# Optimization experiments

Hardware: AMD Instinct MI355X
Metric: run time of the kernel (lower is better)

## Reference

```python
import jax, jax.numpy as jnp
import numpy as np

B_J0 = 0.01
BETA = 1.8   # isAdapt=1
LENS = 0.5
DT = 1.0
IN_SIZE = 1
STRIDE = IN_SIZE
T = 784 // STRIDE
HID = (512, 512, 512)
OUT = 10
N = 256


def _create_general_mask(dim, c_min, c_max, min_dc, max_dc, phase_max, T):
    # faithful port of ASRNN_general.create_general_mask (numpy, static)
    dcs = np.linspace(min_dc, max_dc, dim)
    cycles = np.linspace(c_min, c_max, dim)
    shifts = np.linspace(0.0, float(int(phase_max * c_max)), dim)
    rows = []
    for cyc, dc, ps in zip(cycles, dcs, shifts):
        cyc = int(np.round(cyc))
        on = int(np.round(dc * cyc))
        pat = [1.0] * on + [0.0] * (cyc - on)
        ps = int(np.round(ps))
        if ps > 0:
            pat = pat[-ps:] + pat[:-ps]
        rows.append(pat * (T // cyc) + pat[: T % cyc])
    return np.asarray(rows, dtype=np.float32)  # [dim, T]

MASK1 = jnp.asarray(_create_general_mask(HID[0], 2, 8, 0.2, 0.8, 0.5, T))
MASK2 = jnp.asarray(_create_general_mask(HID[1], 4, 16, 0.2, 0.8, 0.5, T))
MASK3 = jnp.asarray(_create_general_mask(HID[2], 8, 32, 0.2, 0.8, 0.5, T))

# per-step input gather indices (faithful to the start_idx branch in forward)
_starts = np.arange(T) * STRIDE
_IDX = np.where(_starts[:, None] < T - IN_SIZE,
                _starts[:, None] + np.arange(IN_SIZE)[None, :],
                (784 - IN_SIZE) + np.arange(IN_SIZE)[None, :])  # [T, IN]


@jax.custom_vjp
def act_fun(x):
    return (x > 0.0).astype(x.dtype)

def _act_fwd(x):
    return (x > 0.0).astype(x.dtype), x

def _act_bwd(x, g):
    return (g * (jnp.abs(x) < LENS).astype(g.dtype),)

act_fun.defvjp(_act_fwd, _act_bwd)


def _mem_update(inputs, mem, spike, tau_adp, b, tau_m, mask_t):
    alpha = jnp.exp(-DT / tau_m)
    ro = jnp.exp(-DT / tau_adp)
    b_new = ro * b + (1.0 - ro) * spike
    Bth = B_J0 + BETA * b_new
    mem_new = mem * alpha + (1.0 - alpha) * inputs - Bth * spike * DT
    mem_new = jnp.where(mask_t == 0.0, mem, mem_new)
    spike_new = act_fun(mem_new - Bth) * mask_t
    return mem_new, spike_new, b_new


def _forward(x, wi1, bi1, wh1, bh1, wi2, bi2, wh2, bh2, wi3, bi3, wo, bo,
             tau_adp1, tau_adp2, tau_adp3, tau_m1, tau_m2, tau_m3):
    n = x.shape[0]
    x_seq = jnp.transpose(x[:, _IDX], (1, 0, 2))            # [T, N, IN]
    pre1 = jnp.einsum('tni,hi->tnh', x_seq, wi1) + bi1       # [T, N, H1]

    def step_fn(carry, xs):
        mem1, spk1, b1, mem2, spk2, b2, mem3, spk3, b3, out_sum, s1, s2, s3 = carry
        p1, m1, m2, m3 = xs
        h1_in = p1 + spk1 @ wh1.T + bh1
        mem1, spk1, b1 = _mem_update(h1_in, mem1, spk1, tau_adp1, b1, tau_m1, m1)
        h2_in = spk1 @ wi2.T + bi2 + spk2 @ wh2.T + bh2
        mem2, spk2, b2 = _mem_update(h2_in, mem2, spk2, tau_adp2, b2, tau_m2, m2)
        h3_in = spk2 @ wi3.T + bi3
        mem3, spk3, b3 = _mem_update(h3_in, mem3, spk3, tau_adp3, b3, tau_m3, m3)
        out_sum = out_sum + spk3 @ wo.T + bo
        return (mem1, spk1, b1, mem2, spk2, b2, mem3, spk3, b3,
                out_sum, s1 + spk1, s2 + spk2, s3 + spk3), None

    z = lambda h: jnp.zeros((n, h), x.dtype)
    f = lambda h: jnp.full((n, h), B_J0, x.dtype)
    carry0 = (z(HID[0]), z(HID[0]), f(HID[0]),
              z(HID[1]), z(HID[1]), f(HID[1]),
              z(HID[2]), z(HID[2]), f(HID[2]),
              jnp.zeros((n, OUT), x.dtype), z(HID[0]), z(HID[1]), z(HID[2]))
    xs = (pre1, MASK1.T, MASK2.T, MASK3.T)
    carry, _ = jax.lax.scan(step_fn, carry0, xs)
    out_sum, s1, s2, s3 = carry[9], carry[10], carry[11], carry[12]
    outputs = out_sum / T
    layer_fr = jnp.stack([s1.sum() / (n * HID[0] * T),
                          s2.sum() / (n * HID[1] * T),
                          s3.sum() / (n * HID[2] * T)])
    return outputs, s1 / T, s2 / T, s3 / T, layer_fr


def setup_inputs() -> dict:
    key = jax.random.key(0)
    ks = jax.random.split(key, 20)
    def xav(k, shp):
        fan_in, fan_out = shp[1], shp[0]
        s = np.sqrt(2.0 / (fan_in + fan_out))
        return jax.random.normal(k, shp, jnp.float32) * s
    return {
        'x': jax.random.uniform(ks[0], (N, 784), jnp.float32),
        'wi1': xav(ks[1], (HID[0], IN_SIZE)), 'bi1': jnp.zeros((HID[0],), jnp.float32),
        'wh1': xav(ks[2], (HID[0], HID[0])), 'bh1': jnp.zeros((HID[0],), jnp.float32),
        'wi2': xav(ks[3], (HID[1], HID[0])), 'bi2': jnp.zeros((HID[1],), jnp.float32),
        'wh2': xav(ks[4], (HID[1], HID[1])), 'bh2': jnp.zeros((HID[1],), jnp.float32),
        'wi3': xav(ks[5], (HID[2], HID[1])), 'bi3': jnp.zeros((HID[2],), jnp.float32),
        'wo': xav(ks[6], (OUT, HID[2])), 'bo': jnp.zeros((OUT,), jnp.float32),
        'tau_adp1': 700.0 + 25.0 * jax.random.normal(ks[7], (HID[0],), jnp.float32),
        'tau_adp2': 700.0 + 25.0 * jax.random.normal(ks[8], (HID[1],), jnp.float32),
        'tau_adp3': 700.0 + 25.0 * jax.random.normal(ks[9], (HID[2],), jnp.float32),
        'tau_m1': 5.0 + jax.random.normal(ks[10], (HID[0],), jnp.float32),
        'tau_m2': 5.0 + jax.random.normal(ks[11], (HID[1],), jnp.float32),
        'tau_m3': 5.0 + jax.random.normal(ks[12], (HID[2],), jnp.float32),
    }


def reference(x, wi1, bi1, wh1, bh1, wi2, bi2, wh2, bh2, wi3, bi3, wo, bo,
              tau_adp1, tau_adp2, tau_adp3, tau_m1, tau_m2, tau_m3):
    return _forward(x, wi1, bi1, wh1, bh1, wi2, bi2, wh2, bh2, wi3, bi3, wo, bo,
                    tau_adp1, tau_adp2, tau_adp3, tau_m1, tau_m2, tau_m3)
```

## Files before the change

kernel.cpp:

```cpp
#include <hip/hip_runtime.h>
#include <stdint.h>

#pragma clang fp contract(off)


static constexpr int    TS      = 784;
static constexpr size_t WS_WT1  = 0;
static constexpr size_t WS_WT2A = 1u << 20;
static constexpr size_t WS_WT2B = 2u << 20;
static constexpr size_t WS_WT3  = 3u << 20;
static constexpr size_t WS_M1   = 4u << 20;
static constexpr size_t WS_M2   = WS_M1 + (size_t)TS * 512;
static constexpr size_t WS_M3   = WS_M2 + (size_t)TS * 512;
static constexpr size_t WS_FRP  = WS_M3 + (size_t)TS * 512;

__device__ __forceinline__ float exp_np(float x) {
  float q = rintf(x * 1.442695040f);
  float r = __fmaf_rn(-q, 0.693359375f, x);
  r = __fmaf_rn(-q, -2.12194440e-4f, r);
  float r2 = r * r;
  float p = 1.9875691500e-4f;
  p = __fmaf_rn(p, r, 1.3981999507e-3f);
  p = __fmaf_rn(p, r, 8.3334519073e-3f);
  p = __fmaf_rn(p, r, 4.1665795894e-2f);
  p = __fmaf_rn(p, r, 1.6666665459e-1f);
  p = __fmaf_rn(p, r, 5.0000001201e-1f);
  p = __fmaf_rn(p, r2, r);
  p = p + 1.0f;
  return ldexpf(p, (int)q);
}

__device__ __forceinline__ int mask_val(int l, int h, int t) {
  const double cmin = (l == 0) ? 2.0 : ((l == 1) ? 4.0 : 8.0);
  const double cmax = (l == 0) ? 8.0 : ((l == 1) ? 16.0 : 32.0);
  const double smax = (l == 0) ? 4.0 : ((l == 1) ? 8.0 : 16.0);
  const double cD = (cmax - cmin) / 511.0;
  const double dD = (0.8 - 0.2) / 511.0;
  const double sD = smax / 511.0;
  const double hd = (double)h;
  double cycd = (h == 511) ? cmax : __dadd_rn(cmin, __dmul_rn(hd, cD));
  double dcd  = (h == 511) ? 0.8  : __dadd_rn(0.2,  __dmul_rn(hd, dD));
  double psd  = (h == 511) ? smax : __dmul_rn(hd, sD);
  int cyc = __double2int_rn(cycd);
  int on  = __double2int_rn(__dmul_rn(dcd, (double)cyc));
  int ps  = __double2int_rn(psd);
  int eff = (ps >= cyc) ? 0 : ps;
  int pos = (t % cyc) - eff;
  if (pos < 0) pos += cyc;
  return (pos < on) ? 1 : 0;
}

__global__ void setup_masks(char* __restrict__ ws) {
  const int t = blockIdx.x, tid = threadIdx.x;
  uint8_t* m1 = (uint8_t*)(ws + WS_M1);
  uint8_t* m2 = (uint8_t*)(ws + WS_M2);
  uint8_t* m3 = (uint8_t*)(ws + WS_M3);
  for (int h = tid; h < 512; h += 256) {
    m1[t * 512 + h] = (uint8_t)mask_val(0, h, t);
    m2[t * 512 + h] = (uint8_t)mask_val(1, h, t);
    m3[t * 512 + h] = (uint8_t)mask_val(2, h, t);
  }
}

__global__ void transpose_kernel(const float* __restrict__ wh1,
                                 const float* __restrict__ wi2,
                                 const float* __restrict__ wh2,
                                 const float* __restrict__ wi3,
                                 char* __restrict__ ws) {
  const int k = blockIdx.x;
  const int m = blockIdx.y;
  const float* W = (m == 0) ? wh1 : (m == 1) ? wi2 : (m == 2) ? wh2 : wi3;
  float* T = (float*)(ws + (size_t)m * (1u << 20));
  for (int j = threadIdx.x; j < 512; j += 256)
    T[(size_t)k * 512 + j] = W[(size_t)j * 512 + k];
}

__device__ __forceinline__ uint32_t upd32(float hin, uint32_t mk, uint32_t osp,
                                          float al, float om, float r, float omr,
                                          float& memv, float& bv) {
  float t1 = r * bv;
  float bn = osp ? (t1 + omr) : t1;
  float bt = 1.8f * bn;
  float Bth = 0.01f + bt;
  float m1 = memv * al;
  float m2 = om * hin;
  float m3 = m1 + m2;
  float mn = osp ? (m3 - Bth) : m3;
  if (!mk) mn = memv;
  uint32_t sn = (mk && (mn - Bth) > 0.0f) ? 1u : 0u;
  memv = mn; bv = bn;
  return sn;
}

__device__ __forceinline__ int expand_list(const uint64_t* __restrict__ bm,
                                           uint32_t mysp, int h,
                                           ushort* __restrict__ kl) {
  const int wh = h >> 6, bpos = h & 63;
  int cnt = 0, rank = 0;
#pragma unroll
  for (int w = 0; w < 8; ++w) {
    uint64_t v = bm[w];
    int pc = __builtin_popcountll(v);
    if (w < wh) rank += pc;
    cnt += pc;
  }
  rank += __builtin_popcountll(bm[wh] & ((1ull << bpos) - 1ull));
  if (mysp) kl[rank] = (ushort)h;
  return cnt;
}

__device__ __forceinline__ float gather_from(const float* __restrict__ base,
                                             const ushort* kl, int from, int cnt,
                                             float s) {
  int i = from;
  for (; i + 16 <= cnt; i += 16) {
    float w0  = base[(size_t)kl[i + 0]  << 9];
    float w1  = base[(size_t)kl[i + 1]  << 9];
    float w2  = base[(size_t)kl[i + 2]  << 9];
    float w3  = base[(size_t)kl[i + 3]  << 9];
    float w4  = base[(size_t)kl[i + 4]  << 9];
    float w5  = base[(size_t)kl[i + 5]  << 9];
    float w6  = base[(size_t)kl[i + 6]  << 9];
    float w7  = base[(size_t)kl[i + 7]  << 9];
    float w8  = base[(size_t)kl[i + 8]  << 9];
    float w9  = base[(size_t)kl[i + 9]  << 9];
    float w10 = base[(size_t)kl[i + 10] << 9];
    float w11 = base[(size_t)kl[i + 11] << 9];
    float w12 = base[(size_t)kl[i + 12] << 9];
    float w13 = base[(size_t)kl[i + 13] << 9];
    float w14 = base[(size_t)kl[i + 14] << 9];
    float w15 = base[(size_t)kl[i + 15] << 9];
    s = s + w0;  s = s + w1;  s = s + w2;  s = s + w3;
    s = s + w4;  s = s + w5;  s = s + w6;  s = s + w7;
    s = s + w8;  s = s + w9;  s = s + w10; s = s + w11;
    s = s + w12; s = s + w13; s = s + w14; s = s + w15;
  }
  for (; i + 4 <= cnt; i += 4) {
    float w0 = base[(size_t)kl[i + 0] << 9];
    float w1 = base[(size_t)kl[i + 1] << 9];
    float w2 = base[(size_t)kl[i + 2] << 9];
    float w3 = base[(size_t)kl[i + 3] << 9];
    s = s + w0; s = s + w1; s = s + w2; s = s + w3;
  }
  for (; i < cnt; ++i) s = s + base[(size_t)kl[i] << 9];
  return s;
}

__global__ __launch_bounds__(512, 1) void rnn_block(
    const float* __restrict__ x,
    const float* __restrict__ wi1, const float* __restrict__ bi1,
    const float* __restrict__ bh1,
    const float* __restrict__ bi2, const float* __restrict__ bh2,
    const float* __restrict__ bi3,
    const float* __restrict__ wo, const float* __restrict__ bo,
    const float* __restrict__ ta1, const float* __restrict__ ta2,
    const float* __restrict__ ta3, const float* __restrict__ tm1,
    const float* __restrict__ tm2, const float* __restrict__ tm3,
    char* __restrict__ ws, float* __restrict__ d_out) {
  const int n = blockIdx.x;
  const int h = threadIdx.x;
  const float* WT1  = (const float*)(ws + WS_WT1);
  const float* WT2A = (const float*)(ws + WS_WT2A);
  const float* WT2B = (const float*)(ws + WS_WT2B);
  const float* WT3  = (const float*)(ws + WS_WT3);
  const uint8_t* M1 = (const uint8_t*)(ws + WS_M1);
  const uint8_t* M2 = (const uint8_t*)(ws + WS_M2);
  const uint8_t* M3 = (const uint8_t*)(ws + WS_M3);

  __shared__ uint64_t bm1s[8], bm2s[8], bm3s[8];
  __shared__ ushort kl1s[512], kl2s[512];
  __shared__ float woS[10 * 513];
  __shared__ double red[512];

  for (int i = h; i < 5120; i += 512) woS[(i / 512) * 513 + (i % 512)] = wo[i];

  float al1 = exp_np(-1.0f / tm1[h]), om1 = 1.0f - al1;
  float ro1 = exp_np(-1.0f / ta1[h]), omr1 = 1.0f - ro1;
  float al2 = exp_np(-1.0f / tm2[h]), om2 = 1.0f - al2;
  float ro2 = exp_np(-1.0f / ta2[h]), omr2 = 1.0f - ro2;
  float al3 = exp_np(-1.0f / tm3[h]), om3 = 1.0f - al3;
  float ro3 = exp_np(-1.0f / ta3[h]), omr3 = 1.0f - ro3;
  float wi1v = wi1[h], bi1v = bi1[h], bh1v = bh1[h];
  float bi2v = bi2[h], bh2v = bh2[h], bi3v = bi3[h];
  float bo_v = (h < 80 && (h & 7) == 0) ? bo[h >> 3] : 0.0f;

  float mem1 = 0.0f, b1 = 0.01f, c1 = 0.0f;
  float mem2 = 0.0f, b2 = 0.01f, c2 = 0.0f;
  float mem3 = 0.0f, b3 = 0.01f, c3 = 0.0f;
  uint32_t sp1 = 0, sp2 = 0, sp3 = 0;
  int cnt1 = 0, cnt2 = 0;
  float outv = 0.0f;

  const float* xrow = x + (size_t)n * 784;
  __syncthreads();

  for (int t = 0; t < TS; ++t) {
    const uint32_t mk1 = M1[t * 512 + h];
    const uint32_t mk2 = M2[t * 512 + h];
    const uint32_t mk3 = M3[t * 512 + h];
    const float xv = xrow[t];

    float acc1 = 0.0f;
    if (mk1 && cnt1 > 0) acc1 = gather_from(WT1 + h, kl1s, 0, cnt1, 0.0f);
    float p1 = xv * wi1v;
    p1 = p1 + bi1v;
    p1 = p1 + acc1;
    p1 = p1 + bh1v;
    uint32_t sn1 = upd32(p1, mk1, sp1, al1, om1, ro1, omr1, mem1, b1);
    sp1 = sn1; c1 += (float)sn1;
    uint64_t bal1 = __ballot(sn1);
    if ((h & 63) == 0) bm1s[h >> 6] = bal1;
    __syncthreads();
    cnt1 = expand_list(bm1s, sn1, h, kl1s);
    __syncthreads();

    float a1 = 0.0f, a2 = 0.0f;
    if (mk2) {
      const float* bA = WT2A + h;
      const float* bB = WT2B + h;
      int iA = 0, iB = 0;
      while (iA + 8 <= cnt1 && iB + 8 <= cnt2) {
        float wa0 = bA[(size_t)kl1s[iA + 0] << 9];
        float wa1 = bA[(size_t)kl1s[iA + 1] << 9];
        float wa2 = bA[(size_t)kl1s[iA + 2] << 9];
        float wa3 = bA[(size_t)kl1s[iA + 3] << 9];
        float wa4 = bA[(size_t)kl1s[iA + 4] << 9];
        float wa5 = bA[(size_t)kl1s[iA + 5] << 9];
        float wa6 = bA[(size_t)kl1s[iA + 6] << 9];
        float wa7 = bA[(size_t)kl1s[iA + 7] << 9];
        float wb0 = bB[(size_t)kl2s[iB + 0] << 9];
        float wb1 = bB[(size_t)kl2s[iB + 1] << 9];
        float wb2 = bB[(size_t)kl2s[iB + 2] << 9];
        float wb3 = bB[(size_t)kl2s[iB + 3] << 9];
        float wb4 = bB[(size_t)kl2s[iB + 4] << 9];
        float wb5 = bB[(size_t)kl2s[iB + 5] << 9];
        float wb6 = bB[(size_t)kl2s[iB + 6] << 9];
        float wb7 = bB[(size_t)kl2s[iB + 7] << 9];
        a1 = a1 + wa0; a1 = a1 + wa1; a1 = a1 + wa2; a1 = a1 + wa3;
        a1 = a1 + wa4; a1 = a1 + wa5; a1 = a1 + wa6; a1 = a1 + wa7;
        a2 = a2 + wb0; a2 = a2 + wb1; a2 = a2 + wb2; a2 = a2 + wb3;
        a2 = a2 + wb4; a2 = a2 + wb5; a2 = a2 + wb6; a2 = a2 + wb7;
        iA += 8; iB += 8;
      }
      a1 = gather_from(bA, kl1s, iA, cnt1, a1);
      a2 = gather_from(bB, kl2s, iB, cnt2, a2);
    }
    float p2 = a1 + bi2v;
    p2 = p2 + a2;
    p2 = p2 + bh2v;
    uint32_t sn2 = upd32(p2, mk2, sp2, al2, om2, ro2, omr2, mem2, b2);
    sp2 = sn2; c2 += (float)sn2;
    uint64_t bal2 = __ballot(sn2);
    if ((h & 63) == 0) bm2s[h >> 6] = bal2;
    __syncthreads();
    cnt2 = expand_list(bm2s, sn2, h, kl2s);
    __syncthreads();

    float a3 = 0.0f;
    if (mk3 && cnt2 > 0) a3 = gather_from(WT3 + h, kl2s, 0, cnt2, 0.0f);
    float p3 = a3 + bi3v;
    uint32_t sn3 = upd32(p3, mk3, sp3, al3, om3, ro3, omr3, mem3, b3);
    sp3 = sn3; c3 += (float)sn3;
    uint64_t bal3 = __ballot(sn3);
    if ((h & 63) == 0) bm3s[h >> 6] = bal3;
    __syncthreads();

    if (h < 80) {
      const int w = h & 7;
      uint64_t v = bm3s[w];
      float s = 0.0f;
      const float* wrow = &woS[(h >> 3) * 513 + w * 64];
      while (v) { int b = __builtin_ctzll(v); v &= v - 1; s = s + wrow[b]; }
      s += __shfl_down(s, 4, 8);
      s += __shfl_down(s, 2, 8);
      s += __shfl_down(s, 1, 8);
      if (w == 0) { float vv = outv + s; outv = vv + bo_v; }
    }
  }

  d_out[2560 + (size_t)n * 512 + h]          = c1 / 784.0f;
  d_out[2560 + 131072 + (size_t)n * 512 + h] = c2 / 784.0f;
  d_out[2560 + 262144 + (size_t)n * 512 + h] = c3 / 784.0f;
  if (h < 80 && (h & 7) == 0) d_out[(size_t)n * 10 + (h >> 3)] = outv / 784.0f;

  double* FRP = (double*)(ws + WS_FRP);
  red[h] = (double)c1;
  __syncthreads();
  for (int wd = 256; wd > 0; wd >>= 1) {
    if (h < wd) red[h] += red[h + wd];
    __syncthreads();
  }
  if (h == 0) FRP[n * 3 + 0] = red[0];
  __syncthreads();
  red[h] = (double)c2;
  __syncthreads();
  for (int wd = 256; wd > 0; wd >>= 1) {
    if (h < wd) red[h] += red[h + wd];
    __syncthreads();
  }
  if (h == 0) FRP[n * 3 + 1] = red[0];
  __syncthreads();
  red[h] = (double)c3;
  __syncthreads();
  for (int wd = 256; wd > 0; wd >>= 1) {
    if (h < wd) red[h] += red[h + wd];
    __syncthreads();
  }
  if (h == 0) FRP[n * 3 + 2] = red[0];
}

__global__ void finalize_fr(char* __restrict__ ws, float* __restrict__ d_out) {
  const int l = threadIdx.x;
  if (l >= 3) return;
  const double* FRP = (const double*)(ws + WS_FRP);
  double s = 0.0;
  for (int n = 0; n < 256; ++n) s += FRP[n * 3 + l];
  d_out[395776 + l] = (float)(s / (131072.0 * 784.0));
}

extern "C" void kernel_launch(void* const* d_in, const int* in_sizes, int n_in,
                              void* d_out, int out_size, void* d_ws, size_t ws_size,
                              hipStream_t stream) {
  (void)in_sizes; (void)n_in; (void)out_size; (void)ws_size;
  const float* x   = (const float*)d_in[0];
  const float* wi1 = (const float*)d_in[1];
  const float* bi1 = (const float*)d_in[2];
  const float* wh1 = (const float*)d_in[3];
  const float* bh1 = (const float*)d_in[4];
  const float* wi2 = (const float*)d_in[5];
  const float* bi2 = (const float*)d_in[6];
  const float* wh2 = (const float*)d_in[7];
  const float* bh2 = (const float*)d_in[8];
  const float* wi3 = (const float*)d_in[9];
  const float* bi3 = (const float*)d_in[10];
  const float* wo  = (const float*)d_in[11];
  const float* bo  = (const float*)d_in[12];
  const float* ta1 = (const float*)d_in[13];
  const float* ta2 = (const float*)d_in[14];
  const float* ta3 = (const float*)d_in[15];
  const float* tm1 = (const float*)d_in[16];
  const float* tm2 = (const float*)d_in[17];
  const float* tm3 = (const float*)d_in[18];
  char*  ws  = (char*)d_ws;
  float* out = (float*)d_out;

  hipLaunchKernelGGL(setup_masks, dim3(TS), dim3(256), 0, stream, ws);
  hipLaunchKernelGGL(transpose_kernel, dim3(512, 4), dim3(256), 0, stream,
                     wh1, wi2, wh2, wi3, ws);
  hipLaunchKernelGGL(rnn_block, dim3(256), dim3(512), 0, stream,
                     x, wi1, bi1, bh1, bi2, bh2, bi3, wo, bo,
                     ta1, ta2, ta3, tm1, tm2, tm3, ws, out);
  hipLaunchKernelGGL(finalize_fr, dim3(1), dim3(64), 0, stream, ws, out);
}
```

Before: 4.178 ms.

## Hoist next-step layer-1 recurrent gather into layer-3 phase as dual gather

Computes the layer-1 recurrent gather for step t+1 at the end of step t, paired with the layer-3 gather in one interleaved dual-gather loop. This is legal because it only depends on the layer-1 spike list, which is already known by then. It also folds the layer-2 dual gather into a shared helper that uses mask-zeroed counts instead of a branch. The aim is more independent loads in flight per phase and a shorter serial chain in layer 1, at the cost of an extra carried register and a branchless path that may disturb wavefront divergence behaviour.

```diff
diff --git a/kernel.cpp b/kernel.cpp
--- a/kernel.cpp
+++ b/kernel.cpp
@@ -146,6 +146,40 @@
   return s;
 }
 
+__device__ __forceinline__ void dual_gather(
+    const float* __restrict__ bA, const ushort* __restrict__ klA, int cntA,
+    const float* __restrict__ bB, const ushort* __restrict__ klB, int cntB,
+    float& outA, float& outB) {
+  float a = 0.0f, b = 0.0f;
+  int iA = 0, iB = 0;
+  while (iA + 8 <= cntA && iB + 8 <= cntB) {
+    float wa0 = bA[(size_t)klA[iA + 0] << 9];
+    float wa1 = bA[(size_t)klA[iA + 1] << 9];
+    float wa2 = bA[(size_t)klA[iA + 2] << 9];
+    float wa3 = bA[(size_t)klA[iA + 3] << 9];
+    float wa4 = bA[(size_t)klA[iA + 4] << 9];
+    float wa5 = bA[(size_t)klA[iA + 5] << 9];
+    float wa6 = bA[(size_t)klA[iA + 6] << 9];
+    float wa7 = bA[(size_t)klA[iA + 7] << 9];
+    float wb0 = bB[(size_t)klB[iB + 0] << 9];
+    float wb1 = bB[(size_t)klB[iB + 1] << 9];
+    float wb2 = bB[(size_t)klB[iB + 2] << 9];
+    float wb3 = bB[(size_t)klB[iB + 3] << 9];
+    float wb4 = bB[(size_t)klB[iB + 4] << 9];
+    float wb5 = bB[(size_t)klB[iB + 5] << 9];
+    float wb6 = bB[(size_t)klB[iB + 6] << 9];
+    float wb7 = bB[(size_t)klB[iB + 7] << 9];
+    a = a + wa0; a = a + wa1; a = a + wa2; a = a + wa3;
+    a = a + wa4; a = a + wa5; a = a + wa6; a = a + wa7;
+    b = b + wb0; b = b + wb1; b = b + wb2; b = b + wb3;
+    b = b + wb4; b = b + wb5; b = b + wb6; b = b + wb7;
+    iA += 8; iB += 8;
+  }
+  a = gather_from(bA, klA, iA, cntA, a);
+  b = gather_from(bB, klB, iB, cntB, b);
+  outA = a; outB = b;
+}
+
 __global__ __launch_bounds__(512, 1) void rnn_block(
     const float* __restrict__ x,
     const float* __restrict__ wi1, const float* __restrict__ bi1,
@@ -190,18 +224,17 @@
   uint32_t sp1 = 0, sp2 = 0, sp3 = 0;
   int cnt1 = 0, cnt2 = 0;
   float outv = 0.0f;
+  float acc1 = 0.0f;
+  uint32_t mk1 = M1[h];
 
   const float* xrow = x + (size_t)n * 784;
   __syncthreads();
 
   for (int t = 0; t < TS; ++t) {
-    const uint32_t mk1 = M1[t * 512 + h];
     const uint32_t mk2 = M2[t * 512 + h];
     const uint32_t mk3 = M3[t * 512 + h];
     const float xv = xrow[t];
 
-    float acc1 = 0.0f;
-    if (mk1 && cnt1 > 0) acc1 = gather_from(WT1 + h, kl1s, 0, cnt1, 0.0f);
     float p1 = xv * wi1v;
     p1 = p1 + bi1v;
     p1 = p1 + acc1;
@@ -214,36 +247,11 @@
     cnt1 = expand_list(bm1s, sn1, h, kl1s);
     __syncthreads();
 
-    float a1 = 0.0f, a2 = 0.0f;
-    if (mk2) {
-      const float* bA = WT2A + h;
-      const float* bB = WT2B + h;
-      int iA = 0, iB = 0;
-      while (iA + 8 <= cnt1 && iB + 8 <= cnt2) {
-        float wa0 = bA[(size_t)kl1s[iA + 0] << 9];
-        float wa1 = bA[(size_t)kl1s[iA + 1] << 9];
-        float wa2 = bA[(size_t)kl1s[iA + 2] << 9];
-        float wa3 = bA[(size_t)kl1s[iA + 3] << 9];
-        float wa4 = bA[(size_t)kl1s[iA + 4] << 9];
-        float wa5 = bA[(size_t)kl1s[iA + 5] << 9];
-        float wa6 = bA[(size_t)kl1s[iA + 6] << 9];
-        float wa7 = bA[(size_t)kl1s[iA + 7] << 9];
-        float wb0 = bB[(size_t)kl2s[iB + 0] << 9];
-        float wb1 = bB[(size_t)kl2s[iB + 1] << 9];
-        float wb2 = bB[(size_t)kl2s[iB + 2] << 9];
-        float wb3 = bB[(size_t)kl2s[iB + 3] << 9];
-        float wb4 = bB[(size_t)kl2s[iB + 4] << 9];
-        float wb5 = bB[(size_t)kl2s[iB + 5] << 9];
-        float wb6 = bB[(size_t)kl2s[iB + 6] << 9];
-        float wb7 = bB[(size_t)kl2s[iB + 7] << 9];
-        a1 = a1 + wa0; a1 = a1 + wa1; a1 = a1 + wa2; a1 = a1 + wa3;
-        a1 = a1 + wa4; a1 = a1 + wa5; a1 = a1 + wa6; a1 = a1 + wa7;
-        a2 = a2 + wb0; a2 = a2 + wb1; a2 = a2 + wb2; a2 = a2 + wb3;
-        a2 = a2 + wb4; a2 = a2 + wb5; a2 = a2 + wb6; a2 = a2 + wb7;
-        iA += 8; iB += 8;
-      }
-      a1 = gather_from(bA, kl1s, iA, cnt1, a1);
-      a2 = gather_from(bB, kl2s, iB, cnt2, a2);
+    float a1, a2;
+    {
+      const int cA = mk2 ? cnt1 : 0;
+      const int cB = mk2 ? cnt2 : 0;
+      dual_gather(WT2A + h, kl1s, cA, WT2B + h, kl2s, cB, a1, a2);
     }
     float p2 = a1 + bi2v;
     p2 = p2 + a2;
@@ -256,8 +264,15 @@
     cnt2 = expand_list(bm2s, sn2, h, kl2s);
     __syncthreads();
 
-    float a3 = 0.0f;
-    if (mk3 && cnt2 > 0) a3 = gather_from(WT3 + h, kl2s, 0, cnt2, 0.0f);
+    const uint32_t mk1n = (t + 1 < TS) ? M1[(t + 1) * 512 + h] : 0u;
+    float a3, a1n;
+    {
+      const int cG3 = mk3 ? cnt2 : 0;
+      const int cG1 = mk1n ? cnt1 : 0;
+      dual_gather(WT3 + h, kl2s, cG3, WT1 + h, kl1s, cG1, a3, a1n);
+    }
+    acc1 = a1n;
+    mk1 = mk1n;
     float p3 = a3 + bi3v;
     uint32_t sn3 = upd32(p3, mk3, sp3, al3, om3, ro3, omr3, mem3, b3);
     sp3 = sn3; c3 += (float)sn3;
```

New measurement: 4.748 ms. +13.6%, slower.
